# Kernel tuning notes

Hardware: AMD Instinct MI355X
Metric: run time of the kernel (lower is better)

The kernel has to match this reference:

```python
import jax, jax.numpy as jnp
import numpy as np

B, S, D = 2, 2048, 1024
H = 16            # attention heads
KVH = 4           # key/value heads
G = H // KVH      # group_size = 4
HD = D // H       # head_dim = 64
ROPE_THETA = 10000.0


def rope(x):
    # x: [B, S, D]; interleaved-pair rotary embedding over full last dim
    d = x.shape[-1]
    inv_freq = 1.0 / (ROPE_THETA ** (jnp.arange(0, d, 2, dtype=jnp.float32) / d))  # [d/2]
    ang = jnp.arange(x.shape[1], dtype=jnp.float32)[:, None] * inv_freq[None, :]   # [S, d/2]
    cos, sin = jnp.cos(ang), jnp.sin(ang)
    x1, x2 = x[..., 0::2], x[..., 1::2]
    r1 = x1 * cos - x2 * sin
    r2 = x1 * sin + x2 * cos
    out = jnp.stack([r1, r2], axis=-1).reshape(x.shape)
    return out


def setup_inputs() -> dict:
    key = jax.random.key(0)
    kx, kq, kk, kv = jax.random.split(key, 4)
    x = jax.random.normal(kx, (B, S, D), dtype=jnp.float32)
    # mark last 256 positions of batch element 1 as padding via NaN
    x = x.at[1, S - 256:, :].set(jnp.nan)
    scale = 1.0 / np.sqrt(D)
    Wq = jax.random.normal(kq, (D, D), dtype=jnp.float32) * scale
    Wk = jax.random.normal(kk, (D, D // G), dtype=jnp.float32) * scale
    Wv = jax.random.normal(kv, (D, D // G), dtype=jnp.float32) * scale
    return {"x": x, "Wq": Wq, "Wk": Wk, "Wv": Wv}


def reference(x, Wq, Wk, Wv):
    pad = jnp.isnan(x)                      # [B,S,D]
    x = jnp.where(pad, 0.0, x)
    key_pad = jnp.any(pad, axis=-1)         # [B,S] True = padded token

    q = x @ Wq                              # [B,S,D]
    k = jnp.repeat(x @ Wk, G, axis=-1)      # grouped KV, repeat_interleave -> [B,S,D]
    v = jnp.repeat(x @ Wv, G, axis=-1)

    q = rope(q)
    k = rope(k)

    def split_heads(t):
        return t.reshape(B, S, H, HD).transpose(0, 2, 1, 3)  # [B,H,S,HD]

    q, k, v = split_heads(q), split_heads(k), split_heads(v)

    scores = jnp.einsum('bhqd,bhkd->bhqk', q, k) / np.sqrt(HD)
    causal = jnp.tril(jnp.ones((S, S), dtype=bool))
    allow = causal[None, None, :, :] & (~key_pad)[:, None, None, :]
    scores = jnp.where(allow, scores, -1e9)
    attn = jax.nn.softmax(scores, axis=-1)
    out = jnp.einsum('bhqk,bhkd->bhqd', attn, v)
    return out.transpose(0, 2, 1, 3).reshape(B, S, D)
```

## Files before the change

### kernel.cpp

```cpp
#include <hip/hip_runtime.h>
#include <hip/hip_bf16.h>
#include <math.h>

typedef unsigned short u16;
typedef unsigned int u32;
typedef __bf16 bf16x8 __attribute__((ext_vector_type(8)));
typedef float fx4 __attribute__((ext_vector_type(4)));

#define MFMA16(a, b, c) __builtin_amdgcn_mfma_f32_16x16x32_bf16(a, b, c, 0, 0, 0)

static constexpr int Bb = 2, Ss = 2048, Dd = 1024, Hh = 16, DKV = 256;
static constexpr int ROWS = Bb * Ss;
static constexpr float L2T_OVER = 0.0259525632f;
static constexpr float SC2 = 0.18033688f;
static constexpr int PSTR = 76;

__device__ __forceinline__ u16 f2bf(float f) {
    union { float f; u32 i; } v; v.f = f;
    u32 u = v.i;
    return (u16)((u + 0x7FFFu + ((u >> 16) & 1u)) >> 16);
}
__device__ __forceinline__ u16 bfr(float f) {
    return (u16)((__float_as_uint(f) + 0x8000u) >> 16);
}

__device__ __forceinline__ float fexp2(float x) {
    float r; asm("v_exp_f32 %0, %1" : "=v"(r) : "v"(x)); return r;
}
__device__ __forceinline__ void fsincos(float a, float& sn, float& cs) {
    float r = a * 0.15915494309189535f;
    r = r - floorf(r);
    asm("v_sin_f32 %0, %1" : "=v"(sn) : "v"(r));
    asm("v_cos_f32 %0, %1" : "=v"(cs) : "v"(r));
}

__device__ __forceinline__ void gl16(const u16* g, u16* l) {
    __builtin_amdgcn_global_load_lds(
        (const __attribute__((address_space(1))) void*)g,
        (__attribute__((address_space(3))) void*)l, 16, 0, 0);
}

template <int CTRL>
__device__ __forceinline__ float dppf(float x) {
    return __int_as_float(
        __builtin_amdgcn_mov_dpp(__float_as_int(x), CTRL, 0xF, 0xF, true));
}
__device__ __forceinline__ float rsum16(float x) {
    x += dppf<0xB1>(x);
    x += dppf<0x4E>(x);
    x += dppf<0x124>(x);
    x += dppf<0x128>(x);
    return x;
}

__global__ void pre_kernel(const float* __restrict__ x, const float* __restrict__ Wq,
                           const float* __restrict__ Wk, const float* __restrict__ Wv,
                           u16* __restrict__ xc, u32* __restrict__ kpb,
                           u16* __restrict__ wAll) {
    __shared__ u16 tile[32][33];
    __shared__ int flag;
    int bid = blockIdx.x, t = threadIdx.x;
    if (bid < 4096) {
        int row = bid;
        if (t == 0) flag = 0;
        __syncthreads();
        float4 d = *(const float4*)(x + (size_t)row * Dd + t * 4);
        int any = 0;
        float a0 = d.x, a1 = d.y, a2 = d.z, a3 = d.w;
        if ((__float_as_uint(a0) & 0x7FFFFFFFu) > 0x7F800000u) { a0 = 0.f; any = 1; }
        if ((__float_as_uint(a1) & 0x7FFFFFFFu) > 0x7F800000u) { a1 = 0.f; any = 1; }
        if ((__float_as_uint(a2) & 0x7FFFFFFFu) > 0x7F800000u) { a2 = 0.f; any = 1; }
        if ((__float_as_uint(a3) & 0x7FFFFFFFu) > 0x7F800000u) { a3 = 0.f; any = 1; }
        if (any) atomicOr(&flag, 1);
        uint2 o;
        o.x = (u32)f2bf(a0) | ((u32)f2bf(a1) << 16);
        o.y = (u32)f2bf(a2) | ((u32)f2bf(a3) << 16);
        *(uint2*)(xc + (size_t)row * Dd + t * 4) = o;
        __syncthreads();
        if (t == 0 && flag) {
            int b = row >> 11, s = row & (Ss - 1);
            atomicOr(&kpb[b * 64 + (s >> 5)], 1u << (s & 31));
        }
        return;
    }
    const float* in; u16* out; int C, bx, by;
    if (bid < 5120) { int i = bid - 4096; in = Wq; out = wAll; C = Dd; bx = i & 31; by = i >> 5; }
    else if (bid < 5376) { int i = bid - 5120; in = Wk; out = wAll + (size_t)Dd * Dd; C = DKV; bx = i & 7; by = i >> 3; }
    else { int i = bid - 5376; in = Wv; out = wAll + (size_t)1280 * Dd; C = DKV; bx = i & 7; by = i >> 3; }
    int c0 = bx * 32, r0 = by * 32;
    int tx = t & 31, ty = t >> 5;
    for (int i = 0; i < 32; i += 8)
        tile[ty + i][tx] = f2bf(in[(size_t)(r0 + ty + i) * C + c0 + tx]);
    __syncthreads();
    for (int i = 0; i < 32; i += 8)
        out[(size_t)(c0 + ty + i) * Dd + r0 + tx] = tile[tx][ty + i];
}

__global__ __launch_bounds__(256) void gemm_qkv(
    const u16* __restrict__ A, const u16* __restrict__ Bt, u16* __restrict__ qbuf,
    u16* __restrict__ kr, u16* __restrict__ vtb) {
    __shared__ __align__(16) u16 As[2][128 * 32];
    __shared__ __align__(16) u16 Bs[2][64 * 32];
    int t = threadIdx.x, w = t >> 6, lane = t & 63;
    int l15 = lane & 15, quad = lane >> 4;
    int col0 = blockIdx.x * 64, row0 = blockIdx.y * 128;
    int wm = w >> 1, wn = w & 1;
    fx4 acc[4][2];
#pragma unroll
    for (int i = 0; i < 4; ++i)
#pragma unroll
        for (int j = 0; j < 2; ++j) acc[i][j] = (fx4){0.f, 0.f, 0.f, 0.f};

    auto stage = [&](int kb, int buf) {
#pragma unroll
        for (int i = 0; i < 2; ++i) {
            int slot = i * 256 + t;
            int row = slot >> 2, p = slot & 3, g = p ^ ((row >> 1) & 3);
            gl16(A + (size_t)(row0 + row) * Dd + kb * 32 + g * 8,
                 &As[buf][(i * 256 + w * 64) * 8]);
        }
        {
            int row = t >> 2, p = t & 3, g = p ^ ((row >> 1) & 3);
            gl16(Bt + (size_t)(col0 + row) * Dd + kb * 32 + g * 8,
                 &Bs[buf][(w * 64) * 8]);
        }
    };

    stage(0, 0);
    int buf = 0;
    for (int kb = 0; kb < 32; ++kb) {
        __syncthreads();
        if (kb + 1 < 32) stage(kb + 1, buf ^ 1);
        bf16x8 af[4], bf[2];
#pragma unroll
        for (int mi = 0; mi < 4; ++mi) {
            int row = wm * 64 + mi * 16 + l15;
            af[mi] = *(const bf16x8*)(&As[buf][row * 32 + ((quad ^ ((row >> 1) & 3)) * 8)]);
        }
#pragma unroll
        for (int ni = 0; ni < 2; ++ni) {
            int row = wn * 32 + ni * 16 + l15;
            bf[ni] = *(const bf16x8*)(&Bs[buf][row * 32 + ((quad ^ ((row >> 1) & 3)) * 8)]);
        }
#pragma unroll
        for (int mi = 0; mi < 4; ++mi)
#pragma unroll
            for (int ni = 0; ni < 2; ++ni)
                acc[mi][ni] = MFMA16(af[mi], bf[ni], acc[mi][ni]);
        buf ^= 1;
    }

    if (col0 < 1024) {
        bool oddc = (l15 & 1) != 0;
#pragma unroll
        for (int mi = 0; mi < 4; ++mi) {
            int rbase = row0 + wm * 64 + mi * 16 + quad * 4;
#pragma unroll
            for (int ni = 0; ni < 2; ++ni) {
                int ccol = col0 + wn * 32 + ni * 16 + l15;
                float f = fexp2(-(float)(ccol >> 1) * L2T_OVER);
#pragma unroll
                for (int r = 0; r < 4; ++r) {
                    float v = acc[mi][ni][r];
                    float p = dppf<0xB1>(v);
                    float x0 = oddc ? p : v, x1 = oddc ? v : p;
                    float pos = (float)((rbase + r) & (Ss - 1));
                    float sn, cs;
                    fsincos(pos * f, sn, cs);
                    float res = oddc ? (x0 * sn + x1 * cs) : (x0 * cs - x1 * sn);
                    qbuf[(size_t)(rbase + r) * Dd + ccol] = f2bf(res);
                }
            }
        }
    } else if (col0 < 1280) {
#pragma unroll
        for (int mi = 0; mi < 4; ++mi) {
            int rbase = row0 + wm * 64 + mi * 16 + quad * 4;
#pragma unroll
            for (int ni = 0; ni < 2; ++ni) {
                int tt = col0 + wn * 32 + ni * 16 + l15 - 1024;
                float f0 = fexp2(-(float)(2 * tt) * L2T_OVER);
                float f1 = fexp2(-(float)(2 * tt + 1) * L2T_OVER);
#pragma unroll
                for (int r = 0; r < 4; ++r) {
                    int row = rbase + r;
                    float pos = (float)(row & (Ss - 1));
                    float s0, c0, s1, c1;
                    fsincos(pos * f0, s0, c0);
                    fsincos(pos * f1, s1, c1);
                    float kv = acc[mi][ni][r];
                    uint2 o;
                    o.x = (u32)f2bf(kv * (c0 - s0)) | ((u32)f2bf(kv * (s0 + c0)) << 16);
                    o.y = (u32)f2bf(kv * (c1 - s1)) | ((u32)f2bf(kv * (s1 + c1)) << 16);
                    *(uint2*)(kr + (size_t)row * Dd + 4 * tt) = o;
                }
            }
        }
    } else {
#pragma unroll
        for (int mi = 0; mi < 4; ++mi) {
            int rbase = row0 + wm * 64 + mi * 16 + quad * 4;
            int b = rbase >> 11, s0 = rbase & (Ss - 1);
#pragma unroll
            for (int ni = 0; ni < 2; ++ni) {
                int c = col0 + wn * 32 + ni * 16 + l15 - 1280;
                uint2 o;
                o.x = (u32)f2bf(acc[mi][ni][0]) | ((u32)f2bf(acc[mi][ni][1]) << 16);
                o.y = (u32)f2bf(acc[mi][ni][2]) | ((u32)f2bf(acc[mi][ni][3]) << 16);
                *(uint2*)(vtb + (size_t)(b * DKV + c) * Ss + s0) = o;
            }
        }
    }
}

__global__ __launch_bounds__(256) void attn_kernel(
    const u16* __restrict__ qbuf, const u16* __restrict__ kr,
    const u16* __restrict__ vt, const u32* __restrict__ kpb,
    float* __restrict__ O4, float* __restrict__ L4) {
    __shared__ __align__(16) u16 Ks[2][64 * 64];
    __shared__ __align__(16) u16 Ps[4][16 * PSTR];

    int t = threadIdx.x, w = t >> 6, lane = t & 63;
    int l15 = lane & 15, quad = lane >> 4;
    int bid = blockIdx.x;
    int u = bid >> 5, hh = bid & 31;
    int tile, c;
    if (u < 32)      { tile = 24 + (u & 7); c = u >> 3; }
    else if (u < 56) { tile = 16 + ((u - 32) & 7); c = (u - 32) >> 3; }
    else if (u < 72) { tile = 8 + ((u - 56) & 7); c = (u - 56) >> 3; }
    else             { tile = u - 72; c = 0; }
    int b = hh >> 4, h = hh & 15;
    int n = tile + 1, C = (n + 7) >> 3;
    int kb0 = (int)((u32)(n * c) / (u32)C);
    int kbe = (int)((u32)(n * (c + 1)) / (u32)C);
    int q0 = tile * 64;

    int pos = q0 + w * 16 + l15;
    const u16* qp = qbuf + (size_t)(b * Ss + pos) * Dd + h * 64;
    bf16x8 qf0 = *(const bf16x8*)(qp + quad * 8);
    bf16x8 qf1 = *(const bf16x8*)(qp + 32 + quad * 8);

    u32 pw_all = kpb[b * 64 + lane];

    const u16* vrow = vt + (size_t)(b * DKV + h * 16 + l15) * Ss;

    auto stageK = [&](int k0, int buf) {
#pragma unroll
        for (int i2 = 0; i2 < 2; ++i2) {
            int row = i2 * 32 + w * 8 + (lane >> 3);
            int gg = (lane & 7) ^ (row & 7);
            gl16(kr + (size_t)(b * Ss + k0 + row) * Dd + h * 64 + gg * 8,
                 &Ks[buf][(i2 * 32 + w * 8) * 64]);
        }
    };

    float l_lane[4] = {0.f, 0.f, 0.f, 0.f};
    fx4 oacc = (fx4){0.f, 0.f, 0.f, 0.f};

    stageK(kb0 * 64, 0);
    int buf = 0;
    const int qrb = q0 + w * 16 + quad * 4;
    const int qmin = q0 + w * 16;

    for (int kb = kb0; kb < kbe; ++kb) {
        int k0 = kb * 64;
        __syncthreads();
        if (kb + 1 < kbe) stageK(k0 + 64, buf ^ 1);

        bf16x8 vf0 = *(const bf16x8*)(vrow + k0 + quad * 8);
        bf16x8 vf1 = *(const bf16x8*)(vrow + k0 + 32 + quad * 8);

        fx4 s[4];
#pragma unroll
        for (int tt = 0; tt < 4; ++tt) {
            const u16* kb_ = &Ks[buf][(tt * 16 + l15) * 64];
            bf16x8 kf0 = *(const bf16x8*)(kb_ + ((quad ^ (l15 & 7)) * 8));
            bf16x8 kf1 = *(const bf16x8*)(kb_ + (((quad + 4) ^ (l15 & 7)) * 8));
            fx4 z = (fx4){0.f, 0.f, 0.f, 0.f};
            fx4 a = MFMA16(qf0, kf0, z);
            s[tt] = MFMA16(qf1, kf1, a);
        }

        u32 pw0 = (u32)__shfl((int)pw_all, 2 * kb, 64);
        u32 pw1 = (u32)__shfl((int)pw_all, 2 * kb + 1, 64);
        bool fast = (k0 + 63 <= qmin) & ((pw0 | pw1) == 0u);

        float e[4][4];
        if (fast) {
#pragma unroll
            for (int tt = 0; tt < 4; ++tt)
#pragma unroll
                for (int r = 0; r < 4; ++r)
                    e[tt][r] = fexp2(fmaf(s[tt][r], SC2, -32.f));
        } else {
            u32 padb[4];
#pragma unroll
            for (int tt = 0; tt < 4; ++tt)
                padb[tt] = ((tt & 2 ? pw1 : pw0) >> ((tt * 16 + l15) & 31)) & 1u;
#pragma unroll
            for (int r = 0; r < 4; ++r) {
                int qq = qrb + r;
#pragma unroll
                for (int tt = 0; tt < 4; ++tt) {
                    float ee = fexp2(fmaf(s[tt][r], SC2, -32.f));
                    e[tt][r] = (k0 + tt * 16 + l15 <= qq && !padb[tt]) ? ee : 0.f;
                }
            }
        }

#pragma unroll
        for (int r = 0; r < 4; ++r) {
            l_lane[r] += (e[0][r] + e[1][r]) + (e[2][r] + e[3][r]);
            int prow = (quad * 4 + r) * PSTR + l15;
            Ps[w][prow + 0] = bfr(e[0][r]);
            Ps[w][prow + 16] = bfr(e[1][r]);
            Ps[w][prow + 32] = bfr(e[2][r]);
            Ps[w][prow + 48] = bfr(e[3][r]);
        }

        {
            bf16x8 pf0 = *(const bf16x8*)(&Ps[w][l15 * PSTR + quad * 8]);
            bf16x8 pf1 = *(const bf16x8*)(&Ps[w][l15 * PSTR + 32 + quad * 8]);
            oacc = MFMA16(pf0, vf0, oacc);
            oacc = MFMA16(pf1, vf1, oacc);
        }
        buf ^= 1;
    }

#pragma unroll
    for (int r = 0; r < 4; ++r) {
        float l_row = rsum16(l_lane[r]);
        int q = qrb + r;
        size_t slot = ((size_t)hh * Ss + q) * 4 + c;
        O4[slot * 16 + l15] = oacc[r];
        if (l15 == 0) L4[slot] = l_row;
    }
}

__global__ void norm_kernel(const float* __restrict__ O4, const float* __restrict__ L4,
                            float* __restrict__ out) {
    int idx = blockIdx.x * 256 + threadIdx.x;
    int d4 = idx & 255;
    int row = idx >> 8;
    int h = d4 >> 4, f = d4 & 15;
    int b = row >> 11, s = row & (Ss - 1);
    int hh = b * 16 + h;
    int Cn = ((s >> 6) + 8) >> 3;
    size_t base = ((size_t)hh * Ss + s) * 4;
    float o = 0.f, l = 0.f;
    for (int c = 0; c < Cn; ++c) {
        o += O4[(base + c) * 16 + f];
        l += L4[base + c];
    }
    float a = o / l;
    float4 o4 = {a, a, a, a};
    *(float4*)(out + (size_t)row * Dd + d4 * 4) = o4;
}

extern "C" void kernel_launch(void* const* d_in, const int* in_sizes, int n_in,
                              void* d_out, int out_size, void* d_ws, size_t ws_size,
                              hipStream_t stream) {
    const float* x = (const float*)d_in[0];
    const float* Wq = (const float*)d_in[1];
    const float* Wk = (const float*)d_in[2];
    const float* Wv = (const float*)d_in[3];
    float* out = (float*)d_out;

    char* ws = (char*)d_ws;
    const size_t SZ_XC = (size_t)ROWS * Dd * 2;
    const size_t SZ_WALL = (size_t)1536 * Dd * 2;
    const size_t SZ_QB = (size_t)ROWS * Dd * 2;
    const size_t SZ_KR = (size_t)ROWS * Dd * 2;
    const size_t SZ_VTB = (size_t)Bb * DKV * Ss * 2;
    const size_t SZ_KPB = 4096;
    const size_t SZ_O4 = (size_t)32 * Ss * 4 * 16 * 4;
    const size_t SZ_L4 = (size_t)32 * Ss * 4 * 4;

    size_t off = 0;
    u16* xc = (u16*)(ws + off); off += SZ_XC;
    u16* wAll = (u16*)(ws + off); off += SZ_WALL;
    u16* qbuf = (u16*)(ws + off); off += SZ_QB;
    u16* kr = (u16*)(ws + off); off += SZ_KR;
    u16* vtb = (u16*)(ws + off); off += SZ_VTB;
    u32* kpb = (u32*)(ws + off); off += SZ_KPB;
    float* O4 = (float*)(ws + off); off += SZ_O4;
    float* L4 = (float*)(ws + off); off += SZ_L4;
    (void)ws_size; (void)in_sizes; (void)n_in; (void)out_size;

    hipMemsetAsync(kpb, 0, SZ_KPB, stream);
    pre_kernel<<<5632, 256, 0, stream>>>(x, Wq, Wk, Wv, xc, kpb, wAll);
    gemm_qkv<<<dim3(1536 / 64, ROWS / 128), 256, 0, stream>>>(xc, wAll, qbuf, kr, vtb);
    attn_kernel<<<2560, 256, 0, stream>>>(qbuf, kr, vtb, kpb, O4, L4);
    norm_kernel<<<4096, 256, 0, stream>>>(O4, L4, out);
}
```

Measured before the change: 146.3 us.

## Compute transposed scores so P feeds PV MFMA directly from registers

Swaps the QK^T MFMA operands so each lane holds scores for one query across four consecutive keys, which lets the exponentiated probabilities be packed into bf16 registers and fed straight into a 16x16x16 MFMA with V as the A operand. This removes the per-wave LDS staging buffer for P, its writes and reads, and the per-row DPP reductions, replacing them with two cross-lane shuffles for the row sum. It uses twice as many smaller PV MFMAs and narrower V loads, and switches P rounding to round-to-nearest-even, which costs extra ALU work.

```diff
diff --git a/kernel.cpp b/kernel.cpp
--- a/kernel.cpp
+++ b/kernel.cpp
@@ -5,23 +5,25 @@
 typedef unsigned short u16;
 typedef unsigned int u32;
 typedef __bf16 bf16x8 __attribute__((ext_vector_type(8)));
+typedef short s16x4 __attribute__((ext_vector_type(4)));
 typedef float fx4 __attribute__((ext_vector_type(4)));
 
 #define MFMA16(a, b, c) __builtin_amdgcn_mfma_f32_16x16x32_bf16(a, b, c, 0, 0, 0)
+#define MFMAPV(a, b, c) __builtin_amdgcn_mfma_f32_16x16x16bf16_1k(a, b, c, 0, 0, 0)
 
 static constexpr int Bb = 2, Ss = 2048, Dd = 1024, Hh = 16, DKV = 256;
 static constexpr int ROWS = Bb * Ss;
 static constexpr float L2T_OVER = 0.0259525632f;
 static constexpr float SC2 = 0.18033688f;
-static constexpr int PSTR = 76;
 
 __device__ __forceinline__ u16 f2bf(float f) {
     union { float f; u32 i; } v; v.f = f;
     u32 u = v.i;
     return (u16)((u + 0x7FFFu + ((u >> 16) & 1u)) >> 16);
 }
-__device__ __forceinline__ u16 bfr(float f) {
-    return (u16)((__float_as_uint(f) + 0x8000u) >> 16);
+__device__ __forceinline__ u32 f2bfu(float f) {
+    u32 u = __float_as_uint(f);
+    return (u + 0x7FFFu + ((u >> 16) & 1u)) >> 16;
 }
 
 __device__ __forceinline__ float fexp2(float x) {
@@ -44,13 +46,6 @@
 __device__ __forceinline__ float dppf(float x) {
     return __int_as_float(
         __builtin_amdgcn_mov_dpp(__float_as_int(x), CTRL, 0xF, 0xF, true));
-}
-__device__ __forceinline__ float rsum16(float x) {
-    x += dppf<0xB1>(x);
-    x += dppf<0x4E>(x);
-    x += dppf<0x124>(x);
-    x += dppf<0x128>(x);
-    return x;
 }
 
 __global__ void pre_kernel(const float* __restrict__ x, const float* __restrict__ Wq,
@@ -218,7 +213,6 @@
     const u16* __restrict__ vt, const u32* __restrict__ kpb,
     float* __restrict__ O4, float* __restrict__ L4) {
     __shared__ __align__(16) u16 Ks[2][64 * 64];
-    __shared__ __align__(16) u16 Ps[4][16 * PSTR];
 
     int t = threadIdx.x, w = t >> 6, lane = t & 63;
     int l15 = lane & 15, quad = lane >> 4;
@@ -235,8 +229,8 @@
     int kbe = (int)((u32)(n * (c + 1)) / (u32)C);
     int q0 = tile * 64;
 
-    int pos = q0 + w * 16 + l15;
-    const u16* qp = qbuf + (size_t)(b * Ss + pos) * Dd + h * 64;
+    int qq = q0 + w * 16 + l15;
+    const u16* qp = qbuf + (size_t)(b * Ss + qq) * Dd + h * 64;
     bf16x8 qf0 = *(const bf16x8*)(qp + quad * 8);
     bf16x8 qf1 = *(const bf16x8*)(qp + 32 + quad * 8);
 
@@ -254,21 +248,23 @@
         }
     };
 
-    float l_lane[4] = {0.f, 0.f, 0.f, 0.f};
+    float l_lane = 0.f;
     fx4 oacc = (fx4){0.f, 0.f, 0.f, 0.f};
 
     stageK(kb0 * 64, 0);
     int buf = 0;
-    const int qrb = q0 + w * 16 + quad * 4;
     const int qmin = q0 + w * 16;
+    const int kk = quad * 4;
 
     for (int kb = kb0; kb < kbe; ++kb) {
         int k0 = kb * 64;
         __syncthreads();
         if (kb + 1 < kbe) stageK(k0 + 64, buf ^ 1);
 
-        bf16x8 vf0 = *(const bf16x8*)(vrow + k0 + quad * 8);
-        bf16x8 vf1 = *(const bf16x8*)(vrow + k0 + 32 + quad * 8);
+        s16x4 vf[4];
+#pragma unroll
+        for (int tt = 0; tt < 4; ++tt)
+            vf[tt] = *(const s16x4*)(vrow + k0 + tt * 16 + kk);
 
         fx4 s[4];
 #pragma unroll
@@ -277,8 +273,8 @@
             bf16x8 kf0 = *(const bf16x8*)(kb_ + ((quad ^ (l15 & 7)) * 8));
             bf16x8 kf1 = *(const bf16x8*)(kb_ + (((quad + 4) ^ (l15 & 7)) * 8));
             fx4 z = (fx4){0.f, 0.f, 0.f, 0.f};
-            fx4 a = MFMA16(qf0, kf0, z);
-            s[tt] = MFMA16(qf1, kf1, a);
+            fx4 a = MFMA16(kf0, qf0, z);
+            s[tt] = MFMA16(kf1, qf1, a);
         }
 
         u32 pw0 = (u32)__shfl((int)pw_all, 2 * kb, 64);
@@ -293,48 +289,35 @@
                 for (int r = 0; r < 4; ++r)
                     e[tt][r] = fexp2(fmaf(s[tt][r], SC2, -32.f));
         } else {
-            u32 padb[4];
-#pragma unroll
-            for (int tt = 0; tt < 4; ++tt)
-                padb[tt] = ((tt & 2 ? pw1 : pw0) >> ((tt * 16 + l15) & 31)) & 1u;
-#pragma unroll
-            for (int r = 0; r < 4; ++r) {
-                int qq = qrb + r;
-#pragma unroll
-                for (int tt = 0; tt < 4; ++tt) {
+#pragma unroll
+            for (int tt = 0; tt < 4; ++tt) {
+                u32 bits = ((tt & 2) ? pw1 : pw0) >> ((tt * 16 + kk) & 31);
+                int kbase = k0 + tt * 16 + kk;
+#pragma unroll
+                for (int r = 0; r < 4; ++r) {
                     float ee = fexp2(fmaf(s[tt][r], SC2, -32.f));
-                    e[tt][r] = (k0 + tt * 16 + l15 <= qq && !padb[tt]) ? ee : 0.f;
+                    e[tt][r] = (kbase + r <= qq && !((bits >> r) & 1u)) ? ee : 0.f;
                 }
             }
         }
 
 #pragma unroll
-        for (int r = 0; r < 4; ++r) {
-            l_lane[r] += (e[0][r] + e[1][r]) + (e[2][r] + e[3][r]);
-            int prow = (quad * 4 + r) * PSTR + l15;
-            Ps[w][prow + 0] = bfr(e[0][r]);
-            Ps[w][prow + 16] = bfr(e[1][r]);
-            Ps[w][prow + 32] = bfr(e[2][r]);
-            Ps[w][prow + 48] = bfr(e[3][r]);
-        }
-
-        {
-            bf16x8 pf0 = *(const bf16x8*)(&Ps[w][l15 * PSTR + quad * 8]);
-            bf16x8 pf1 = *(const bf16x8*)(&Ps[w][l15 * PSTR + 32 + quad * 8]);
-            oacc = MFMA16(pf0, vf0, oacc);
-            oacc = MFMA16(pf1, vf1, oacc);
+        for (int tt = 0; tt < 4; ++tt) {
+            l_lane += (e[tt][0] + e[tt][1]) + (e[tt][2] + e[tt][3]);
+            union { u32 uu[2]; s16x4 v; } pk;
+            pk.uu[0] = f2bfu(e[tt][0]) | (f2bfu(e[tt][1]) << 16);
+            pk.uu[1] = f2bfu(e[tt][2]) | (f2bfu(e[tt][3]) << 16);
+            oacc = MFMAPV(vf[tt], pk.v, oacc);
         }
         buf ^= 1;
     }
 
-#pragma unroll
-    for (int r = 0; r < 4; ++r) {
-        float l_row = rsum16(l_lane[r]);
-        int q = qrb + r;
-        size_t slot = ((size_t)hh * Ss + q) * 4 + c;
-        O4[slot * 16 + l15] = oacc[r];
-        if (l15 == 0) L4[slot] = l_row;
-    }
+    float l_red = l_lane;
+    l_red += __shfl_xor(l_red, 16, 64);
+    l_red += __shfl_xor(l_red, 32, 64);
+    size_t slot = ((size_t)hh * Ss + qq) * 4 + c;
+    *(fx4*)(&O4[slot * 16 + kk]) = oacc;
+    if (lane < 16) L4[slot] = l_red;
 }
 
 __global__ void norm_kernel(const float* __restrict__ O4, const float* __restrict__ L4,
```

Result: slower. 159.0 us (+8.7%).

## Double attention query tile to 128 rows per block to reuse staged K/V

Applied to the files above, without the earlier changes.

Each attention block now covers 128 query rows instead of 64. Each wave holds two 16-row Q fragments and reuses every staged K tile and V fragment for both, so the K global-to-LDS traffic per query row is halved. The tile-to-split schedule, the per-split key ranges and the norm kernel's split count are updated to match, and the grid is halved. The trade-off is more registers per wave and half as many blocks, which can lower occupancy and load balance. The diagonal blocks also do more masked work.

```diff
diff --git a/kernel.cpp b/kernel.cpp
--- a/kernel.cpp
+++ b/kernel.cpp
@@ -218,27 +218,30 @@
     const u16* __restrict__ vt, const u32* __restrict__ kpb,
     float* __restrict__ O4, float* __restrict__ L4) {
     __shared__ __align__(16) u16 Ks[2][64 * 64];
-    __shared__ __align__(16) u16 Ps[4][16 * PSTR];
+    __shared__ __align__(16) u16 Ps[4][2][16 * PSTR];
 
     int t = threadIdx.x, w = t >> 6, lane = t & 63;
     int l15 = lane & 15, quad = lane >> 4;
     int bid = blockIdx.x;
     int u = bid >> 5, hh = bid & 31;
-    int tile, c;
-    if (u < 32)      { tile = 24 + (u & 7); c = u >> 3; }
-    else if (u < 56) { tile = 16 + ((u - 32) & 7); c = (u - 32) >> 3; }
-    else if (u < 72) { tile = 8 + ((u - 56) & 7); c = (u - 56) >> 3; }
-    else             { tile = u - 72; c = 0; }
+    int tq, c;
+    if (u < 16)      { tq = 12 + (u & 3); c = u >> 2; }
+    else if (u < 28) { int v = u - 16; tq = 8 + (v & 3); c = v >> 2; }
+    else if (u < 36) { int v = u - 28; tq = 4 + (v & 3); c = v >> 2; }
+    else             { tq = 3 - (u - 36); c = 0; }
     int b = hh >> 4, h = hh & 15;
-    int n = tile + 1, C = (n + 7) >> 3;
+    int n = 2 * tq + 2, C = (n + 7) >> 3;
     int kb0 = (int)((u32)(n * c) / (u32)C);
     int kbe = (int)((u32)(n * (c + 1)) / (u32)C);
-    int q0 = tile * 64;
-
-    int pos = q0 + w * 16 + l15;
-    const u16* qp = qbuf + (size_t)(b * Ss + pos) * Dd + h * 64;
-    bf16x8 qf0 = *(const bf16x8*)(qp + quad * 8);
-    bf16x8 qf1 = *(const bf16x8*)(qp + 32 + quad * 8);
+    int q0 = tq * 128;
+
+    bf16x8 qf0[2], qf1[2];
+#pragma unroll
+    for (int m = 0; m < 2; ++m) {
+        const u16* qp = qbuf + (size_t)(b * Ss + q0 + w * 32 + m * 16 + l15) * Dd + h * 64;
+        qf0[m] = *(const bf16x8*)(qp + quad * 8);
+        qf1[m] = *(const bf16x8*)(qp + 32 + quad * 8);
+    }
 
     u32 pw_all = kpb[b * 64 + lane];
 
@@ -254,13 +257,14 @@
         }
     };
 
-    float l_lane[4] = {0.f, 0.f, 0.f, 0.f};
-    fx4 oacc = (fx4){0.f, 0.f, 0.f, 0.f};
+    float l_lane[2][4] = {{0.f, 0.f, 0.f, 0.f}, {0.f, 0.f, 0.f, 0.f}};
+    fx4 oacc[2];
+    oacc[0] = (fx4){0.f, 0.f, 0.f, 0.f};
+    oacc[1] = (fx4){0.f, 0.f, 0.f, 0.f};
 
     stageK(kb0 * 64, 0);
     int buf = 0;
-    const int qrb = q0 + w * 16 + quad * 4;
-    const int qmin = q0 + w * 16;
+    const int qmin = q0 + w * 32;
 
     for (int kb = kb0; kb < kbe; ++kb) {
         int k0 = kb * 64;
@@ -270,71 +274,78 @@
         bf16x8 vf0 = *(const bf16x8*)(vrow + k0 + quad * 8);
         bf16x8 vf1 = *(const bf16x8*)(vrow + k0 + 32 + quad * 8);
 
-        fx4 s[4];
+        u32 pw0 = (u32)__shfl((int)pw_all, 2 * kb, 64);
+        u32 pw1 = (u32)__shfl((int)pw_all, 2 * kb + 1, 64);
+        bool fast = (k0 + 63 <= qmin) & ((pw0 | pw1) == 0u);
+
+        fx4 s[2][4];
 #pragma unroll
         for (int tt = 0; tt < 4; ++tt) {
             const u16* kb_ = &Ks[buf][(tt * 16 + l15) * 64];
             bf16x8 kf0 = *(const bf16x8*)(kb_ + ((quad ^ (l15 & 7)) * 8));
             bf16x8 kf1 = *(const bf16x8*)(kb_ + (((quad + 4) ^ (l15 & 7)) * 8));
-            fx4 z = (fx4){0.f, 0.f, 0.f, 0.f};
-            fx4 a = MFMA16(qf0, kf0, z);
-            s[tt] = MFMA16(qf1, kf1, a);
-        }
-
-        u32 pw0 = (u32)__shfl((int)pw_all, 2 * kb, 64);
-        u32 pw1 = (u32)__shfl((int)pw_all, 2 * kb + 1, 64);
-        bool fast = (k0 + 63 <= qmin) & ((pw0 | pw1) == 0u);
-
-        float e[4][4];
-        if (fast) {
-#pragma unroll
-            for (int tt = 0; tt < 4; ++tt)
-#pragma unroll
-                for (int r = 0; r < 4; ++r)
-                    e[tt][r] = fexp2(fmaf(s[tt][r], SC2, -32.f));
-        } else {
-            u32 padb[4];
-#pragma unroll
-            for (int tt = 0; tt < 4; ++tt)
-                padb[tt] = ((tt & 2 ? pw1 : pw0) >> ((tt * 16 + l15) & 31)) & 1u;
+#pragma unroll
+            for (int m = 0; m < 2; ++m) {
+                fx4 z = (fx4){0.f, 0.f, 0.f, 0.f};
+                fx4 a = MFMA16(qf0[m], kf0, z);
+                s[m][tt] = MFMA16(qf1[m], kf1, a);
+            }
+        }
+
+#pragma unroll
+        for (int m = 0; m < 2; ++m) {
+            const int qrb = q0 + w * 32 + m * 16 + quad * 4;
+            float e[4][4];
+            if (fast) {
+#pragma unroll
+                for (int tt = 0; tt < 4; ++tt)
+#pragma unroll
+                    for (int r = 0; r < 4; ++r)
+                        e[tt][r] = fexp2(fmaf(s[m][tt][r], SC2, -32.f));
+            } else {
+                u32 padb[4];
+#pragma unroll
+                for (int tt = 0; tt < 4; ++tt)
+                    padb[tt] = ((tt & 2 ? pw1 : pw0) >> ((tt * 16 + l15) & 31)) & 1u;
+#pragma unroll
+                for (int r = 0; r < 4; ++r) {
+                    int qq = qrb + r;
+#pragma unroll
+                    for (int tt = 0; tt < 4; ++tt) {
+                        float ee = fexp2(fmaf(s[m][tt][r], SC2, -32.f));
+                        e[tt][r] = (k0 + tt * 16 + l15 <= qq && !padb[tt]) ? ee : 0.f;
+                    }
+                }
+            }
+
 #pragma unroll
             for (int r = 0; r < 4; ++r) {
-                int qq = qrb + r;
-#pragma unroll
-                for (int tt = 0; tt < 4; ++tt) {
-                    float ee = fexp2(fmaf(s[tt][r], SC2, -32.f));
-                    e[tt][r] = (k0 + tt * 16 + l15 <= qq && !padb[tt]) ? ee : 0.f;
-                }
-            }
-        }
-
+                l_lane[m][r] += (e[0][r] + e[1][r]) + (e[2][r] + e[3][r]);
+                int prow = (quad * 4 + r) * PSTR + l15;
+                Ps[w][m][prow + 0] = bfr(e[0][r]);
+                Ps[w][m][prow + 16] = bfr(e[1][r]);
+                Ps[w][m][prow + 32] = bfr(e[2][r]);
+                Ps[w][m][prow + 48] = bfr(e[3][r]);
+            }
+
+            bf16x8 pf0 = *(const bf16x8*)(&Ps[w][m][l15 * PSTR + quad * 8]);
+            bf16x8 pf1 = *(const bf16x8*)(&Ps[w][m][l15 * PSTR + 32 + quad * 8]);
+            oacc[m] = MFMA16(pf0, vf0, oacc[m]);
+            oacc[m] = MFMA16(pf1, vf1, oacc[m]);
+        }
+        buf ^= 1;
+    }
+
+#pragma unroll
+    for (int m = 0; m < 2; ++m)
 #pragma unroll
         for (int r = 0; r < 4; ++r) {
-            l_lane[r] += (e[0][r] + e[1][r]) + (e[2][r] + e[3][r]);
-            int prow = (quad * 4 + r) * PSTR + l15;
-            Ps[w][prow + 0] = bfr(e[0][r]);
-            Ps[w][prow + 16] = bfr(e[1][r]);
-            Ps[w][prow + 32] = bfr(e[2][r]);
-            Ps[w][prow + 48] = bfr(e[3][r]);
-        }
-
-        {
-            bf16x8 pf0 = *(const bf16x8*)(&Ps[w][l15 * PSTR + quad * 8]);
-            bf16x8 pf1 = *(const bf16x8*)(&Ps[w][l15 * PSTR + 32 + quad * 8]);
-            oacc = MFMA16(pf0, vf0, oacc);
-            oacc = MFMA16(pf1, vf1, oacc);
-        }
-        buf ^= 1;
-    }
-
-#pragma unroll
-    for (int r = 0; r < 4; ++r) {
-        float l_row = rsum16(l_lane[r]);
-        int q = qrb + r;
-        size_t slot = ((size_t)hh * Ss + q) * 4 + c;
-        O4[slot * 16 + l15] = oacc[r];
-        if (l15 == 0) L4[slot] = l_row;
-    }
+            float l_row = rsum16(l_lane[m][r]);
+            int q = q0 + w * 32 + m * 16 + quad * 4 + r;
+            size_t slot = ((size_t)hh * Ss + q) * 4 + c;
+            O4[slot * 16 + l15] = oacc[m][r];
+            if (l15 == 0) L4[slot] = l_row;
+        }
 }
 
 __global__ void norm_kernel(const float* __restrict__ O4, const float* __restrict__ L4,
@@ -345,7 +356,7 @@
     int h = d4 >> 4, f = d4 & 15;
     int b = row >> 11, s = row & (Ss - 1);
     int hh = b * 16 + h;
-    int Cn = ((s >> 6) + 8) >> 3;
+    int Cn = (2 * (s >> 7) + 9) >> 3;
     size_t base = ((size_t)hh * Ss + s) * 4;
     float o = 0.f, l = 0.f;
     for (int c = 0; c < Cn; ++c) {
@@ -390,6 +401,6 @@
     hipMemsetAsync(kpb, 0, SZ_KPB, stream);
     pre_kernel<<<5632, 256, 0, stream>>>(x, Wq, Wk, Wv, xc, kpb, wAll);
     gemm_qkv<<<dim3(1536 / 64, ROWS / 128), 256, 0, stream>>>(xc, wAll, qbuf, kr, vtb);
-    attn_kernel<<<2560, 256, 0, stream>>>(qbuf, kr, vtb, kpb, O4, L4);
+    attn_kernel<<<1280, 256, 0, stream>>>(qbuf, kr, vtb, kpb, O4, L4);
     norm_kernel<<<4096, 256, 0, stream>>>(O4, L4, out);
 }
```

Measured after the change: 145.9 us. Within noise of the previous version (-0.3%).
